# Performance work log

Hardware: AMD Instinct MI355X
Metric: run time of the kernel (lower is better)

Reference implementation:

```python
import jax, jax.numpy as jnp
import numpy as np

B, T, I, H = 32, 8192, 16, 128
G = 3 * H  # gru gate dim
LN_EPS = 1e-5


def _ln(v):
    # LayerNorm over last dim, elementwise_affine=False
    m = jnp.mean(v, axis=-1, keepdims=True)
    var = jnp.mean(jnp.square(v - m), axis=-1, keepdims=True)
    return (v - m) * jax.lax.rsqrt(var + LN_EPS)


def setup_inputs() -> dict:
    key = jax.random.key(0)
    ks = jax.random.split(key, 10)
    std = 1.0 / np.sqrt(H)
    u = lambda k, shape: jax.random.uniform(k, shape, jnp.float32, -std, std)
    return {
        "xs": jax.random.normal(ks[0], (B, T, I), jnp.float32),
        "state": jax.random.normal(ks[1], (1, B, H), jnp.float32),
        "alpha_i": jax.random.normal(ks[2], (B, G), jnp.float32),
        "beta_i": jax.random.normal(ks[3], (B, G), jnp.float32),
        "alpha_h": jax.random.normal(ks[4], (B, G), jnp.float32),
        "beta_h": jax.random.normal(ks[5], (B, G), jnp.float32),
        "Wx": u(ks[6], (G, I)),
        "bx": u(ks[7], (G,)),
        "Wh": u(ks[8], (G, H)),
        "bh": u(ks[9], (G,)),
    }


def reference(xs, state, alpha_i, beta_i, alpha_h, beta_h, Wx, bx, Wh, bh):
    h0 = state[0]  # [B, H]  (rearrange '1 b h -> b 1 h' then squeeze the step dim)
    # Input projection + LayerNorm + FiLM is independent of the recurrence -> batch over T.
    ih_all = _ln(jnp.einsum('bti,gi->btg', xs, Wx) + bx)
    ih_all = ih_all * alpha_i[:, None, :] + beta_i[:, None, :]  # [B, T, 3H]

    def step(h, ih):
        hh = _ln(h @ Wh.T + bh) * alpha_h + beta_h  # [B, 3H]
        i_r, i_i, i_n = jnp.split(ih, 3, axis=-1)
        h_r, h_i, h_n = jnp.split(hh, 3, axis=-1)
        resetgate = jax.nn.sigmoid(i_r + h_r)
        inputgate = jax.nn.sigmoid(i_i + h_i)
        newgate = jnp.tanh(i_n + resetgate * h_n)
        hy = newgate + inputgate * (h - newgate)
        return hy, hy

    hT, ys = jax.lax.scan(step, h0, jnp.swapaxes(ih_all, 0, 1))  # scan over T
    outputs = jnp.swapaxes(ys, 0, 1)  # [B, T, H]
    return outputs, hT[:, None, :]  # state as [B, 1, H] like the torch module
```

## Files before the change

### kernel.cpp

```cpp
#include <hip/hip_runtime.h>


#define T_STEPS 8192
#define BATCH   32
#define HDIM    128
#define GDIM    384
#define IDIM    16
#define LN_EPS  1e-5f
#define NT      512

typedef float f32x2 __attribute__((ext_vector_type(2)));
typedef float f32x4 __attribute__((ext_vector_type(4)));

__device__ __forceinline__ void block_barrier() {
  asm volatile("s_waitcnt lgkmcnt(0)\n\ts_barrier" ::: "memory");
}

__device__ __forceinline__ float fast_sigmoid(float x) {
  return 1.f / (1.f + __expf(-x));
}
__device__ __forceinline__ float fast_tanh(float x) {
  float e2 = __expf(2.f * x);
  return 1.f - 2.f / (e2 + 1.f);
}
__device__ __forceinline__ float hsum4(f32x4 v) {
  return (v.x + v.y) + (v.z + v.w);
}

template <int CTRL>
__device__ __forceinline__ float dppadd(float x) {
  return x + __int_as_float(
      __builtin_amdgcn_update_dpp(0, __float_as_int(x), CTRL, 0xF, 0xF, true));
}
__device__ __forceinline__ float dpp_sum16(float x) {
  x = dppadd<0xB1>(x);
  x = dppadd<0x4E>(x);
  x = dppadd<0x141>(x);
  x = dppadd<0x140>(x);
  return x;
}
__device__ __forceinline__ float qcomb(float v) {
  v += __shfl_xor(v, 16);
  v += __shfl_xor(v, 32);
  return v;
}

#define HPAD (HDIM + 12)

__global__ __launch_bounds__(NT, 2) void gru_v4(
    const float* __restrict__ xs,
    const float* __restrict__ state,
    const float* __restrict__ alpha_i,
    const float* __restrict__ beta_i,
    const float* __restrict__ alpha_h,
    const float* __restrict__ beta_h,
    const float* __restrict__ Wx,
    const float* __restrict__ bx,
    const float* __restrict__ Wh,
    const float* __restrict__ bh,
    float* __restrict__ out)
{
  __shared__ float lds_h[HPAD];
  __shared__ __align__(16) f32x4 lds_stat[8];

  const int b    = blockIdx.x;
  const int tid  = threadIdx.x;
  const int w    = tid >> 6;
  const int lane = tid & 63;
  const int q    = lane >> 4;
  const int j    = w * 16 + (lane & 15);

  const int rowR = j, rowI = j + HDIM, rowN = j + 2 * HDIM;

  f32x4 wr[8], wi[8], wn[8];
  {
    const f32x4* pr = (const f32x4*)(Wh + (size_t)rowR * HDIM + q * 32);
    const f32x4* pi = (const f32x4*)(Wh + (size_t)rowI * HDIM + q * 32);
    const f32x4* pn = (const f32x4*)(Wh + (size_t)rowN * HDIM + q * 32);
#pragma unroll
    for (int k = 0; k < 8; ++k) {
      wr[k] = pr[k]; wi[k] = pi[k]; wn[k] = pn[k];
      asm volatile("" : "+v"(wr[k]), "+v"(wi[k]), "+v"(wn[k]));
    }
  }
  f32x4 wxr = ((const f32x4*)(Wx + (size_t)rowR * IDIM))[q];
  f32x4 wxi = ((const f32x4*)(Wx + (size_t)rowI * IDIM))[q];
  f32x4 wxn = ((const f32x4*)(Wx + (size_t)rowN * IDIM))[q];
  asm volatile("" : "+v"(wxr), "+v"(wxi), "+v"(wxn));

  const float bh_r = bh[rowR], bh_i = bh[rowI], bh_n = bh[rowN];
  const float bx_r = bx[rowR], bx_i = bx[rowI], bx_n = bx[rowN];
  const float ah_r = alpha_h[b * GDIM + rowR];
  const float ah_i = alpha_h[b * GDIM + rowI];
  const float ah_n = alpha_h[b * GDIM + rowN];
  const float bt_r = beta_h[b * GDIM + rowR];
  const float bt_i = beta_h[b * GDIM + rowI];
  const float bt_n = beta_h[b * GDIM + rowN];
  const float ai_r = alpha_i[b * GDIM + rowR];
  const float ai_i = alpha_i[b * GDIM + rowI];
  const float ai_n = alpha_i[b * GDIM + rowN];
  const float bi_r = beta_i[b * GDIM + rowR];
  const float bi_i = beta_i[b * GDIM + rowI];
  const float bi_n = beta_i[b * GDIM + rowN];

  float hreg = state[b * HDIM + j];
  if (lane < 16) lds_h[j + ((j >> 5) << 2)] = hreg;

  const f32x4* xp = (const f32x4*)(xs + (size_t)b * T_STEPS * IDIM);
  float* out_b = out + (size_t)b * T_STEPS * HDIM;

  f32x4 xA = xp[q], xB = xp[4 + q];

  const float invd = 1.f / (float)GDIM;

#define STEP(tcur, X)                                                          \
  do {                                                                         \
    block_barrier();                                       \
    const f32x4* hb = (const f32x4*)(lds_h + q * 36);                          \
    f32x4 ar0 = {0.f, 0.f, 0.f, 0.f}, ar1 = ar0;                               \
    f32x4 ai0 = ar0, ai1 = ar0, an0 = ar0, an1 = ar0;                          \
    _Pragma("unroll") for (int k = 0; k < 8; k += 2) {                         \
      f32x4 h0 = hb[k], h1 = hb[k + 1];                                        \
      ar0 = __builtin_elementwise_fma(wr[k], h0, ar0);                         \
      ar1 = __builtin_elementwise_fma(wr[k + 1], h1, ar1);                     \
      ai0 = __builtin_elementwise_fma(wi[k], h0, ai0);                         \
      ai1 = __builtin_elementwise_fma(wi[k + 1], h1, ai1);                     \
      an0 = __builtin_elementwise_fma(wn[k], h0, an0);                         \
      an1 = __builtin_elementwise_fma(wn[k + 1], h1, an1);                     \
    }                                                                          \
    float accr = hsum4(ar0 + ar1);                                             \
    float acci = hsum4(ai0 + ai1);                                             \
    float accn = hsum4(an0 + an1);                                             \
    f32x4 z = {0.f, 0.f, 0.f, 0.f};                                            \
    float aJr = hsum4(__builtin_elementwise_fma(wxr, X, z));                   \
    float aJi = hsum4(__builtin_elementwise_fma(wxi, X, z));                   \
    float aJn = hsum4(__builtin_elementwise_fma(wxn, X, z));                   \
    float Ar = qcomb(accr) + bh_r;                                             \
    float Ai = qcomb(acci) + bh_i;                                             \
    float An = qcomb(accn) + bh_n;                                             \
    float Jr = qcomb(aJr) + bx_r;                                              \
    float Ji = qcomb(aJi) + bx_i;                                              \
    float Jn = qcomb(aJn) + bx_n;                                              \
    f32x4 st = {Ar + Ai + An, Ar * Ar + Ai * Ai + An * An,                     \
                Jr + Ji + Jn, Jr * Jr + Ji * Ji + Jn * Jn};                    \
    st.x = dpp_sum16(st.x); st.y = dpp_sum16(st.y);                            \
    st.z = dpp_sum16(st.z); st.w = dpp_sum16(st.w);                            \
    if (lane == 0) lds_stat[w] = st;                                           \
    block_barrier();                                   \
    f32x4 sT = ((lds_stat[0] + lds_stat[1]) + (lds_stat[2] + lds_stat[3])) +   \
               ((lds_stat[4] + lds_stat[5]) + (lds_stat[6] + lds_stat[7]));    \
    float mH = sT.x * invd;                                                    \
    float rH = rsqrtf(sT.y * invd - mH * mH + LN_EPS);                         \
    float mI = sT.z * invd;                                                    \
    float rI = rsqrtf(sT.w * invd - mI * mI + LN_EPS);                         \
    float hhr = (Ar - mH) * rH * ah_r + bt_r;                                  \
    float hhi = (Ai - mH) * rH * ah_i + bt_i;                                  \
    float hhn = (An - mH) * rH * ah_n + bt_n;                                  \
    float ihr = (Jr - mI) * rI * ai_r + bi_r;                                  \
    float ihi = (Ji - mI) * rI * ai_i + bi_i;                                  \
    float ihn = (Jn - mI) * rI * ai_n + bi_n;                                  \
    float rg = fast_sigmoid(ihr + hhr);                                        \
    float ig = fast_sigmoid(ihi + hhi);                                        \
    float ng = fast_tanh(ihn + rg * hhn);                                      \
    float hy = ng + ig * (hreg - ng);                                          \
    hreg = hy;                                                                 \
    if (lane < 16) {                                                           \
      lds_h[j + ((j >> 5) << 2)] = hy;                                         \
      out_b[(size_t)(tcur) * HDIM + j] = hy;                                   \
    }                                                                          \
    int tn = (tcur) + 2 < T_STEPS ? (tcur) + 2 : T_STEPS - 1;                  \
    X = xp[(size_t)tn * 4 + q];                                                \
  } while (0)

  for (int t = 0; t < T_STEPS; t += 2) {
    STEP(t, xA);
    STEP(t + 1, xB);
  }
#undef STEP

  if (lane < 16)
    out[(size_t)BATCH * T_STEPS * HDIM + b * HDIM + j] = hreg;
}

extern "C" void kernel_launch(void* const* d_in, const int* in_sizes, int n_in,
                              void* d_out, int out_size, void* d_ws, size_t ws_size,
                              hipStream_t stream) {
  const float* xs      = (const float*)d_in[0];
  const float* state   = (const float*)d_in[1];
  const float* alpha_i = (const float*)d_in[2];
  const float* beta_i  = (const float*)d_in[3];
  const float* alpha_h = (const float*)d_in[4];
  const float* beta_h  = (const float*)d_in[5];
  const float* Wx      = (const float*)d_in[6];
  const float* bx      = (const float*)d_in[7];
  const float* Wh      = (const float*)d_in[8];
  const float* bh      = (const float*)d_in[9];
  float* out = (float*)d_out;

  gru_v4<<<dim3(BATCH), dim3(NT), 0, stream>>>(
      xs, state, alpha_i, beta_i, alpha_h, beta_h, Wx, bx, Wh, bh, out);
}
```

Baseline: 11.09 ms.

## Split input projection into separate kernel and use split-bf16 MFMA recurrence

Adds a parallel kernel that precomputes the input projection, LayerNorm and FiLM for all timesteps into workspace. The recurrent kernel then runs 256 threads per batch row and computes h@Wh^T with bf16 MFMA, splitting both h and W into hi/lo parts (three MFMAs per tile) to keep near-fp32 accuracy. The aim is to cut the per-step latency of the serial recurrence. In exchange it reads a large precomputed activation tensor every step, adds a barrier per step, and runs three times the matrix work. The old kernel remains as a fallback when the workspace is too small.

```diff
diff --git a/kernel.cpp b/kernel.cpp
--- a/kernel.cpp
+++ b/kernel.cpp
@@ -7,15 +7,14 @@
 #define GDIM    384
 #define IDIM    16
 #define LN_EPS  1e-5f
-#define NT      512
 
 typedef float f32x2 __attribute__((ext_vector_type(2)));
 typedef float f32x4 __attribute__((ext_vector_type(4)));
+typedef short bf16x8 __attribute__((ext_vector_type(8)));
 
 __device__ __forceinline__ void block_barrier() {
   asm volatile("s_waitcnt lgkmcnt(0)\n\ts_barrier" ::: "memory");
 }
-
 __device__ __forceinline__ float fast_sigmoid(float x) {
   return 1.f / (1.f + __expf(-x));
 }
@@ -23,8 +22,13 @@
   float e2 = __expf(2.f * x);
   return 1.f - 2.f / (e2 + 1.f);
 }
-__device__ __forceinline__ float hsum4(f32x4 v) {
-  return (v.x + v.y) + (v.z + v.w);
+__device__ __forceinline__ unsigned short f2bf(float x) {
+  unsigned u = __float_as_uint(x);
+  u += 0x7FFFu + ((u >> 16) & 1u);
+  return (unsigned short)(u >> 16);
+}
+__device__ __forceinline__ float bf2f(unsigned short h) {
+  return __uint_as_float(((unsigned)h) << 16);
 }
 
 template <int CTRL>
@@ -39,37 +43,241 @@
   x = dppadd<0x140>(x);
   return x;
 }
+
+__global__ __launch_bounds__(256) void inproj(
+    const float* __restrict__ xs, const float* __restrict__ alpha_i,
+    const float* __restrict__ beta_i, const float* __restrict__ Wx,
+    const float* __restrict__ bx, float* __restrict__ ih_all) {
+  const int wid = threadIdx.x >> 6;
+  const int lane = threadIdx.x & 63;
+  const size_t w = (size_t)blockIdx.x * 4 + wid;
+  const int b = (int)(w >> 13);
+  const f32x4* xp = (const f32x4*)(xs + w * IDIM);
+  f32x4 x0 = xp[0], x1 = xp[1], x2 = xp[2], x3 = xp[3];
+
+  float acc[6];
+  float s = 0.f, s2 = 0.f;
+#pragma unroll
+  for (int k = 0; k < 6; ++k) {
+    const int g = k * 64 + lane;
+    const f32x4* wp = (const f32x4*)(Wx + (size_t)g * IDIM);
+    f32x4 a = __builtin_elementwise_fma(wp[0], x0, (f32x4){0.f, 0.f, 0.f, 0.f});
+    a = __builtin_elementwise_fma(wp[1], x1, a);
+    a = __builtin_elementwise_fma(wp[2], x2, a);
+    a = __builtin_elementwise_fma(wp[3], x3, a);
+    float v = bx[g] + ((a.x + a.y) + (a.z + a.w));
+    acc[k] = v;
+    s += v;
+    s2 += v * v;
+  }
+  s = dpp_sum16(s);  s2 = dpp_sum16(s2);
+  s += __shfl_xor(s, 16);  s2 += __shfl_xor(s2, 16);
+  s += __shfl_xor(s, 32);  s2 += __shfl_xor(s2, 32);
+
+  const float inv = 1.f / (float)GDIM;
+  const float m = s * inv;
+  const float r = rsqrtf(s2 * inv - m * m + LN_EPS);
+
+  float* op = ih_all + w * GDIM;
+  const float* ai = alpha_i + (size_t)b * GDIM;
+  const float* bi = beta_i + (size_t)b * GDIM;
+#pragma unroll
+  for (int k = 0; k < 6; ++k) {
+    const int g = k * 64 + lane;
+    op[g] = (acc[k] - m) * r * ai[g] + bi[g];
+  }
+}
+
+__global__ __launch_bounds__(256, 1) void gru_mfma(
+    const float* __restrict__ state,
+    const float* __restrict__ alpha_h,
+    const float* __restrict__ beta_h,
+    const float* __restrict__ Wh,
+    const float* __restrict__ bh,
+    const float* __restrict__ ih_all,
+    float* __restrict__ out)
+{
+  __shared__ __align__(16) unsigned short lds_hhi[HDIM];
+  __shared__ __align__(16) unsigned short lds_hlo[HDIM];
+  __shared__ __align__(16) f32x2 lds_stat[4];
+
+  const int b    = blockIdx.x;
+  const int tid  = threadIdx.x;
+  const int w    = tid >> 6;
+  const int lane = tid & 63;
+  const int c16  = lane & 15;
+  const int kg   = lane >> 4;
+  const int j0   = 32 * w + c16;
+
+  int rows[6];
+#pragma unroll
+  for (int g3 = 0; g3 < 3; ++g3) {
+#pragma unroll
+    for (int sub = 0; sub < 2; ++sub)
+      rows[g3 * 2 + sub] = g3 * HDIM + 32 * w + sub * 16 + c16;
+  }
+
+  bf16x8 Bhi[6][4], Blo[6][4];
+#pragma unroll
+  for (int tt = 0; tt < 6; ++tt) {
+#pragma unroll
+    for (int c = 0; c < 4; ++c) {
+      const float* wp = Wh + (size_t)rows[tt] * HDIM + c * 32 + kg * 8;
+      f32x4 w0 = ((const f32x4*)wp)[0];
+      f32x4 w1 = ((const f32x4*)wp)[1];
+      bf16x8 hi, lo;
+#pragma unroll
+      for (int e = 0; e < 4; ++e) {
+        unsigned short h0 = f2bf(w0[e]);
+        hi[e] = (short)h0;
+        lo[e] = (short)f2bf(w0[e] - bf2f(h0));
+      }
+#pragma unroll
+      for (int e = 0; e < 4; ++e) {
+        unsigned short h0 = f2bf(w1[e]);
+        hi[4 + e] = (short)h0;
+        lo[4 + e] = (short)f2bf(w1[e] - bf2f(h0));
+      }
+      Bhi[tt][c] = hi;
+      Blo[tt][c] = lo;
+    }
+  }
+
+  float bhv[6], ahv[6], btv[6];
+#pragma unroll
+  for (int tt = 0; tt < 6; ++tt) {
+    bhv[tt] = bh[rows[tt]];
+    ahv[tt] = alpha_h[b * GDIM + rows[tt]];
+    btv[tt] = beta_h[b * GDIM + rows[tt]];
+  }
+
+  float h0 = state[b * HDIM + j0];
+  float h1 = state[b * HDIM + j0 + 16];
+  if (lane < 16) {
+    unsigned short hh0 = f2bf(h0), hh1 = f2bf(h1);
+    lds_hhi[j0] = hh0;
+    lds_hhi[j0 + 16] = hh1;
+    lds_hlo[j0] = f2bf(h0 - bf2f(hh0));
+    lds_hlo[j0 + 16] = f2bf(h1 - bf2f(hh1));
+  }
+
+  const float* ih_b = ih_all + (size_t)b * T_STEPS * GDIM;
+  float* out_b = out + (size_t)b * T_STEPS * HDIM;
+
+  float ihA[6], ihB[6];
+#pragma unroll
+  for (int tt = 0; tt < 6; ++tt) {
+    ihA[tt] = ih_b[rows[tt]];
+    ihB[tt] = ih_b[GDIM + rows[tt]];
+  }
+
+  const float invd = 1.f / (float)GDIM;
+  block_barrier();
+
+#define STEP(tcur, IH, H0, H1)                                                 \
+  do {                                                                         \
+          \
+    bf16x8 Ahi[4], Alo[4];                                                     \
+    _Pragma("unroll") for (int c = 0; c < 4; ++c) {                            \
+      Ahi[c] = *(const bf16x8*)(&lds_hhi[c * 32 + kg * 8]);                    \
+      Alo[c] = *(const bf16x8*)(&lds_hlo[c * 32 + kg * 8]);                    \
+    }                                                                          \
+    f32x4 C[6];                                                                \
+    _Pragma("unroll") for (int tt = 0; tt < 6; ++tt)                           \
+        C[tt] = (f32x4){0.f, 0.f, 0.f, 0.f};                                   \
+    _Pragma("unroll") for (int c = 0; c < 4; ++c) {                            \
+      _Pragma("unroll") for (int tt = 0; tt < 6; ++tt) {                       \
+        C[tt] = __builtin_amdgcn_mfma_f32_16x16x32_bf16(Ahi[c], Bhi[tt][c],    \
+                                                        C[tt], 0, 0, 0);       \
+        C[tt] = __builtin_amdgcn_mfma_f32_16x16x32_bf16(Alo[c], Bhi[tt][c],    \
+                                                        C[tt], 0, 0, 0);       \
+        C[tt] = __builtin_amdgcn_mfma_f32_16x16x32_bf16(Ahi[c], Blo[tt][c],    \
+                                                        C[tt], 0, 0, 0);       \
+      }                                                                        \
+    }                                                                          \
+    float acc[6];                                                              \
+    float s = 0.f, s2 = 0.f;                                                   \
+    _Pragma("unroll") for (int tt = 0; tt < 6; ++tt) {                         \
+      acc[tt] = C[tt][0] + bhv[tt];                                            \
+      s += acc[tt];                                                            \
+      s2 += acc[tt] * acc[tt];                                                 \
+    }                                                                          \
+    s = dpp_sum16(s);                                                          \
+    s2 = dpp_sum16(s2);                                                        \
+    if (lane == 0) lds_stat[w] = (f32x2){s, s2};                               \
+    block_barrier();                             \
+    f32x4 p0 = *(const f32x4*)&lds_stat[0];                                    \
+    f32x4 p1 = *(const f32x4*)&lds_stat[2];                                    \
+    float S = (p0.x + p0.z) + (p1.x + p1.z);                                   \
+    float S2 = (p0.y + p0.w) + (p1.y + p1.w);                                  \
+    float mH = S * invd;                                                       \
+    float rH = rsqrtf(S2 * invd - mH * mH + LN_EPS);                           \
+    float hh[6];                                                               \
+    _Pragma("unroll") for (int tt = 0; tt < 6; ++tt)                           \
+        hh[tt] = (acc[tt] - mH) * rH * ahv[tt] + btv[tt];                      \
+    float rg0 = fast_sigmoid(IH[0] + hh[0]);                                   \
+    float rg1 = fast_sigmoid(IH[1] + hh[1]);                                   \
+    float ig0 = fast_sigmoid(IH[2] + hh[2]);                                   \
+    float ig1 = fast_sigmoid(IH[3] + hh[3]);                                   \
+    float ng0 = fast_tanh(IH[4] + rg0 * hh[4]);                                \
+    float ng1 = fast_tanh(IH[5] + rg1 * hh[5]);                                \
+    float hy0 = ng0 + ig0 * (H0 - ng0);                                        \
+    float hy1 = ng1 + ig1 * (H1 - ng1);                                        \
+    H0 = hy0;                                                                  \
+    H1 = hy1;                                                                  \
+    if (lane < 16) {                                                           \
+      unsigned short q0 = f2bf(hy0), q1 = f2bf(hy1);                           \
+      lds_hhi[j0] = q0;                                                        \
+      lds_hhi[j0 + 16] = q1;                                                   \
+      lds_hlo[j0] = f2bf(hy0 - bf2f(q0));                                      \
+      lds_hlo[j0 + 16] = f2bf(hy1 - bf2f(q1));                                 \
+      out_b[(size_t)(tcur)*HDIM + j0] = hy0;                                   \
+      out_b[(size_t)(tcur)*HDIM + j0 + 16] = hy1;                              \
+    }                                                                          \
+    int tn = (tcur) + 2 < T_STEPS ? (tcur) + 2 : T_STEPS - 1;                  \
+    const float* pp = ih_b + (size_t)tn * GDIM;                                \
+    _Pragma("unroll") for (int tt = 0; tt < 6; ++tt) IH[tt] = pp[rows[tt]];    \
+    block_barrier();                                          \
+  } while (0)
+
+  for (int t = 0; t < T_STEPS; t += 2) {
+    STEP(t, ihA, h0, h1);
+    STEP(t + 1, ihB, h0, h1);
+  }
+#undef STEP
+
+  if (lane < 16) {
+    out[(size_t)BATCH * T_STEPS * HDIM + b * HDIM + j0] = h0;
+    out[(size_t)BATCH * T_STEPS * HDIM + b * HDIM + j0 + 16] = h1;
+  }
+}
+
+#define NT 512
+#define HPAD (HDIM + 12)
 __device__ __forceinline__ float qcomb(float v) {
   v += __shfl_xor(v, 16);
   v += __shfl_xor(v, 32);
   return v;
 }
-
-#define HPAD (HDIM + 12)
-
+__device__ __forceinline__ float hsum4(f32x4 v) {
+  return (v.x + v.y) + (v.z + v.w);
+}
 __global__ __launch_bounds__(NT, 2) void gru_v4(
-    const float* __restrict__ xs,
-    const float* __restrict__ state,
-    const float* __restrict__ alpha_i,
-    const float* __restrict__ beta_i,
-    const float* __restrict__ alpha_h,
-    const float* __restrict__ beta_h,
-    const float* __restrict__ Wx,
-    const float* __restrict__ bx,
-    const float* __restrict__ Wh,
-    const float* __restrict__ bh,
-    float* __restrict__ out)
-{
+    const float* __restrict__ xs, const float* __restrict__ state,
+    const float* __restrict__ alpha_i, const float* __restrict__ beta_i,
+    const float* __restrict__ alpha_h, const float* __restrict__ beta_h,
+    const float* __restrict__ Wx, const float* __restrict__ bx,
+    const float* __restrict__ Wh, const float* __restrict__ bh,
+    float* __restrict__ out) {
   __shared__ float lds_h[HPAD];
   __shared__ __align__(16) f32x4 lds_stat[8];
 
-  const int b    = blockIdx.x;
-  const int tid  = threadIdx.x;
-  const int w    = tid >> 6;
+  const int b = blockIdx.x;
+  const int tid = threadIdx.x;
+  const int w = tid >> 6;
   const int lane = tid & 63;
-  const int q    = lane >> 4;
-  const int j    = w * 16 + (lane & 15);
-
+  const int q = lane >> 4;
+  const int j = w * 16 + (lane & 15);
   const int rowR = j, rowI = j + HDIM, rowN = j + 2 * HDIM;
 
   f32x4 wr[8], wi[8], wn[8];
@@ -108,14 +316,12 @@
 
   const f32x4* xp = (const f32x4*)(xs + (size_t)b * T_STEPS * IDIM);
   float* out_b = out + (size_t)b * T_STEPS * HDIM;
-
   f32x4 xA = xp[q], xB = xp[4 + q];
-
   const float invd = 1.f / (float)GDIM;
 
-#define STEP(tcur, X)                                                          \
+#define STEP4(tcur, X)                                                         \
   do {                                                                         \
-    block_barrier();                                       \
+    block_barrier();                                                           \
     const f32x4* hb = (const f32x4*)(lds_h + q * 36);                          \
     f32x4 ar0 = {0.f, 0.f, 0.f, 0.f}, ar1 = ar0;                               \
     f32x4 ai0 = ar0, ai1 = ar0, an0 = ar0, an1 = ar0;                          \
@@ -146,7 +352,7 @@
     st.x = dpp_sum16(st.x); st.y = dpp_sum16(st.y);                            \
     st.z = dpp_sum16(st.z); st.w = dpp_sum16(st.w);                            \
     if (lane == 0) lds_stat[w] = st;                                           \
-    block_barrier();                                   \
+    block_barrier();                                                           \
     f32x4 sT = ((lds_stat[0] + lds_stat[1]) + (lds_stat[2] + lds_stat[3])) +   \
                ((lds_stat[4] + lds_stat[5]) + (lds_stat[6] + lds_stat[7]));    \
     float mH = sT.x * invd;                                                    \
@@ -166,17 +372,17 @@
     hreg = hy;                                                                 \
     if (lane < 16) {                                                           \
       lds_h[j + ((j >> 5) << 2)] = hy;                                         \
-      out_b[(size_t)(tcur) * HDIM + j] = hy;                                   \
+      out_b[(size_t)(tcur)*HDIM + j] = hy;                                     \
     }                                                                          \
     int tn = (tcur) + 2 < T_STEPS ? (tcur) + 2 : T_STEPS - 1;                  \
     X = xp[(size_t)tn * 4 + q];                                                \
   } while (0)
 
   for (int t = 0; t < T_STEPS; t += 2) {
-    STEP(t, xA);
-    STEP(t + 1, xB);
-  }
-#undef STEP
+    STEP4(t, xA);
+    STEP4(t + 1, xB);
+  }
+#undef STEP4
 
   if (lane < 16)
     out[(size_t)BATCH * T_STEPS * HDIM + b * HDIM + j] = hreg;
@@ -197,6 +403,15 @@
   const float* bh      = (const float*)d_in[9];
   float* out = (float*)d_out;
 
-  gru_v4<<<dim3(BATCH), dim3(NT), 0, stream>>>(
-      xs, state, alpha_i, beta_i, alpha_h, beta_h, Wx, bx, Wh, bh, out);
-}
+  const size_t ih_bytes = (size_t)BATCH * T_STEPS * GDIM * sizeof(float);
+  if (ws_size >= ih_bytes) {
+    float* ih_all = (float*)d_ws;
+    inproj<<<dim3(BATCH * T_STEPS / 4), dim3(256), 0, stream>>>(
+        xs, alpha_i, beta_i, Wx, bx, ih_all);
+    gru_mfma<<<dim3(BATCH), dim3(256), 0, stream>>>(
+        state, alpha_h, beta_h, Wh, bh, ih_all, out);
+  } else {
+    gru_v4<<<dim3(BATCH), dim3(NT), 0, stream>>>(
+        xs, state, alpha_i, beta_i, alpha_h, beta_h, Wx, bx, Wh, bh, out);
+  }
+}
```

After: 9.604 ms. 1.16x faster.
